# Kernel tuning notes

Measured on AMD Instinct MI355X. Metric: run time of the kernel, lower is better.

## Reference

```python
import jax, jax.numpy as jnp
import numpy as np

B, LC, LQ, D = 16, 1024, 128, 512


def setup_inputs() -> dict:
    key = jax.random.key(0)
    k1, k2, k3, k4, k5 = jax.random.split(key, 5)
    return {
        "C": jax.random.normal(k1, (B, LC, D), dtype=jnp.float32),
        "Q": jax.random.normal(k2, (B, LQ, D), dtype=jnp.float32),
        "Cmask": jax.random.randint(k3, (B, LC), 0, 2, dtype=jnp.int32),
        "Qmask": jax.random.randint(k4, (B, LQ), 0, 2, dtype=jnp.int32),
        "w_sim": jax.random.normal(k5, (3 * D,), dtype=jnp.float32) * (1.0 / np.sqrt(3 * D)),
    }


def reference(C, Q, Cmask, Qmask, w_sim):
    d = C.shape[-1]
    # Decompose Linear(3d -> 1) on cat([C_rep, Q_rep, C*Q]) into three dot products:
    # S[b,i,j] = C[b,i].w1 + Q[b,j].w2 + (C[b,i]*Q[b,j]).w3
    w1, w2, w3 = w_sim[:d], w_sim[d:2 * d], w_sim[2 * d:]
    s_c = C @ w1                                    # (B, Lc)
    s_q = Q @ w2                                    # (B, Lq)
    s_cq = jnp.einsum('bid,bjd->bij', C * w3, Q)    # (B, Lc, Lq)
    S = s_c[:, :, None] + s_q[:, None, :] + s_cq    # (B, Lc, Lq)

    NEG = jnp.asarray(-1e10, S.dtype)
    S1 = jax.nn.softmax(jnp.where(Qmask[:, None, :] != 0, NEG, S), axis=2)  # over question
    S2 = jax.nn.softmax(jnp.where(Cmask[:, :, None] != 0, NEG, S), axis=1)  # over context

    A = jnp.einsum('bij,bjd->bid', S1, Q)                       # (B, Lc, d)
    # bmm(bmm(S1, S2^T), C) == S1 @ (S2^T @ C) (associativity, avoids Lc x Lc)
    S2tC = jnp.einsum('bij,bid->bjd', S2, C)                    # (B, Lq, d)
    Bv = jnp.einsum('bij,bjd->bid', S1, S2tC)                   # (B, Lc, d)

    # dropout treated as identity (eval / p-effective 0) for the reference
    return jnp.concatenate([C, A, C * A, C * Bv], axis=2)       # (B, Lc, 4d)
```

## Files before the change

### kernel.cpp

```cpp
#include <hip/hip_runtime.h>
#include <hip/hip_bf16.h>
#include <math.h>

#define NB 16
#define NLC 1024
#define NLQ 128
#define ND 512
#define NEGV (-1.0e10f)

typedef __attribute__((ext_vector_type(8))) short bf16x8f;
typedef __attribute__((ext_vector_type(4))) float f32x4a;

__device__ inline unsigned short f2bf(float f) {
    unsigned u = __float_as_uint(f);
    unsigned r = (u + 0x7fffu + ((u >> 16) & 1u)) >> 16;
    return (unsigned short)r;
}

__device__ inline int xcd_swz(int bid, int nwg) {
    int chunk = nwg >> 3;
    return (bid & 7) * chunk + (bid >> 3);
}

__global__ __launch_bounds__(512) void k_prep2(const float* __restrict__ C,
                                               const float* __restrict__ Q,
                                               const float* __restrict__ w,
                                               unsigned short* __restrict__ Cw3,
                                               unsigned short* __restrict__ Ct,
                                               unsigned short* __restrict__ Qb,
                                               unsigned short* __restrict__ Qt,
                                               float* __restrict__ sc,
                                               float* __restrict__ sq) {
    __shared__ float T[64][65];
    int x = blockIdx.x, t = threadIdx.x;
    const float* src; const float* wdot; const float* wmul;
    unsigned short* rout; unsigned short* tout; float* sdst;
    int rows;
    if (x < 256) {
        int b = x >> 4, r0t = (x & 15) * 64;
        src = C + ((size_t)b * NLC + r0t) * ND;
        wdot = w; wmul = w + 2 * ND;
        rout = Cw3 + ((size_t)b * NLC + r0t) * ND;
        tout = Ct + (size_t)b * ND * NLC + r0t;
        sdst = sc + b * NLC + r0t;
        rows = NLC;
    } else {
        int x2 = x - 256;
        int b = x2 >> 1, r0t = (x2 & 1) * 64;
        src = Q + ((size_t)b * NLQ + r0t) * ND;
        wdot = w + ND; wmul = nullptr;
        rout = Qb + ((size_t)b * NLQ + r0t) * ND;
        tout = Qt + (size_t)b * ND * NLQ + r0t;
        sdst = sq + b * NLQ + r0t;
        rows = NLQ;
    }
    int r = t >> 3;
    int s8 = (t & 7) * 8;
    float dacc = 0.f;
    for (int c = 0; c < 8; ++c) {
        int dbase = c * 64 + s8;
        float4 v0 = *(const float4*)&src[(size_t)r * ND + dbase];
        float4 v1 = *(const float4*)&src[(size_t)r * ND + dbase + 4];
        float4 wd0 = *(const float4*)&wdot[dbase];
        float4 wd1 = *(const float4*)&wdot[dbase + 4];
        dacc += v0.x * wd0.x + v0.y * wd0.y + v0.z * wd0.z + v0.w * wd0.w;
        dacc += v1.x * wd1.x + v1.y * wd1.y + v1.z * wd1.z + v1.w * wd1.w;
        float f8[8] = {v0.x, v0.y, v0.z, v0.w, v1.x, v1.y, v1.z, v1.w};
        unsigned short o[8];
        if (wmul) {
            float4 w30 = *(const float4*)&wmul[dbase];
            float4 w31 = *(const float4*)&wmul[dbase + 4];
            float m8[8] = {w30.x, w30.y, w30.z, w30.w, w31.x, w31.y, w31.z, w31.w};
#pragma unroll
            for (int e = 0; e < 8; ++e) o[e] = f2bf(f8[e] * m8[e]);
        } else {
#pragma unroll
            for (int e = 0; e < 8; ++e) o[e] = f2bf(f8[e]);
        }
        *(int4*)&rout[(size_t)r * ND + dbase] = *(int4*)o;
#pragma unroll
        for (int e = 0; e < 8; ++e) T[r][s8 + e] = f8[e];
        __syncthreads();
        {
            int dd = t >> 3, seg = (t & 7) * 8;
            unsigned short o16[8];
#pragma unroll
            for (int e = 0; e < 8; ++e) o16[e] = f2bf(T[seg + e][dd]);
            *(int4*)&tout[(size_t)(c * 64 + dd) * rows + seg] = *(int4*)o16;
        }
        __syncthreads();
    }
    dacc += __shfl_xor(dacc, 1, 64);
    dacc += __shfl_xor(dacc, 2, 64);
    dacc += __shfl_xor(dacc, 4, 64);
    if ((t & 7) == 0) sdst[r] = dacc;
}

__global__ __launch_bounds__(256) void k_S(const unsigned short* __restrict__ Cw3,
                                           const unsigned short* __restrict__ Qb,
                                           const float* __restrict__ sc,
                                           const float* __restrict__ sq,
                                           const int* __restrict__ Qmask,
                                           const int* __restrict__ Cmask,
                                           unsigned short* __restrict__ P1,
                                           unsigned short* __restrict__ Eb,
                                           float* __restrict__ colm,
                                           float* __restrict__ cols) {
    __shared__ __align__(16) char lds[25088];
    int lg = xcd_swz(blockIdx.x, 256);
    int b = lg >> 4, it = lg & 15, i0 = it * 64;
    int t = threadIdx.x, lane = t & 63, wv = t >> 6;
    int g = lane >> 4, r16 = lane & 15;
    const unsigned short* Asrc = Cw3 + ((size_t)b * NLC + i0) * ND;
    const unsigned short* Bsrc = Qb + (size_t)b * NLQ * ND;
    f32x4a zero = {0.f, 0.f, 0.f, 0.f};
    f32x4a acc[8];
#pragma unroll
    for (int nf = 0; nf < 8; ++nf) acc[nf] = zero;

    for (int kk = 0; kk < 8; ++kk) {
#pragma unroll
        for (int p = 0; p < 2; ++p) {
            int u = t + p * 256;
            int i = u >> 3, db = u & 7;
            int4 v = *(const int4*)(Asrc + (size_t)i * ND + kk * 64 + db * 8);
            *(int4*)(lds + i * 128 + ((db * 16) ^ ((i & 7) << 4))) = v;
        }
#pragma unroll
        for (int p = 0; p < 4; ++p) {
            int u = t + p * 256;
            int j = u >> 3, db = u & 7;
            int4 v = *(const int4*)(Bsrc + (size_t)j * ND + kk * 64 + db * 8);
            *(int4*)(lds + 8192 + j * 128 + ((db * 16) ^ ((j & 7) << 4))) = v;
        }
        __syncthreads();
#pragma unroll
        for (int ks = 0; ks < 2; ++ks) {
            int inner = ks * 64 + g * 16;
            bf16x8f a = *(const bf16x8f*)(lds + (16 * wv + r16) * 128 + (inner ^ ((r16 & 7) << 4)));
#pragma unroll
            for (int nf = 0; nf < 8; ++nf) {
                bf16x8f bq = *(const bf16x8f*)(lds + 8192 + (16 * nf + r16) * 128 + (inner ^ ((r16 & 7) << 4)));
                acc[nf] = __builtin_amdgcn_mfma_f32_16x16x32_bf16(a, bq, acc[nf], 0, 0, 0);
            }
        }
        __syncthreads();
    }

    const float* scp = sc + b * NLC + i0;
    const float* sqp = sq + b * NLQ;
    const int* qm = Qmask + b * NLQ;
    const int* cmb = Cmask + b * NLC;
    float sv[8][4];
    float scr[4];
#pragma unroll
    for (int reg = 0; reg < 4; ++reg) scr[reg] = scp[16 * wv + 4 * g + reg];
    int qmv[8];
#pragma unroll
    for (int nf = 0; nf < 8; ++nf) {
        qmv[nf] = qm[16 * nf + r16];
        float sqv = sqp[16 * nf + r16];
#pragma unroll
        for (int reg = 0; reg < 4; ++reg) sv[nf][reg] = acc[nf][reg] + scr[reg] + sqv;
    }

    unsigned short* P1p = P1 + ((size_t)b * NLC + i0) * NLQ;
#pragma unroll
    for (int reg = 0; reg < 4; ++reg) {
        float m = -INFINITY;
#pragma unroll
        for (int nf = 0; nf < 8; ++nf) m = fmaxf(m, qmv[nf] ? NEGV : sv[nf][reg]);
#pragma unroll
        for (int off = 8; off >= 1; off >>= 1) m = fmaxf(m, __shfl_xor(m, off, 64));
        float pv[8], s = 0.f;
#pragma unroll
        for (int nf = 0; nf < 8; ++nf) {
            pv[nf] = __expf((qmv[nf] ? NEGV : sv[nf][reg]) - m);
            s += pv[nf];
        }
#pragma unroll
        for (int off = 8; off >= 1; off >>= 1) s += __shfl_xor(s, off, 64);
        float rsi = 1.0f / s;
        int i = 16 * wv + 4 * g + reg;
#pragma unroll
        for (int nf = 0; nf < 8; ++nf)
            P1p[(size_t)i * NLQ + 16 * nf + r16] = f2bf(pv[nf] * rsi);
    }

    int cmv[4];
#pragma unroll
    for (int reg = 0; reg < 4; ++reg) cmv[reg] = cmb[i0 + 16 * wv + 4 * g + reg];
    float vm2[8][4];
#pragma unroll
    for (int nf = 0; nf < 8; ++nf)
#pragma unroll
        for (int reg = 0; reg < 4; ++reg) vm2[nf][reg] = cmv[reg] ? NEGV : sv[nf][reg];

    float* cpm = (float*)(lds + 20480);
    float* cps = (float*)(lds + 22528);
    float* mtl = (float*)(lds + 24576);
    float cm8[8], cs8[8];
#pragma unroll
    for (int nf = 0; nf < 8; ++nf) {
        float m = vm2[nf][0];
#pragma unroll
        for (int reg = 1; reg < 4; ++reg) m = fmaxf(m, vm2[nf][reg]);
        float s = 0.f;
#pragma unroll
        for (int reg = 0; reg < 4; ++reg) s += __expf(vm2[nf][reg] - m);
#pragma unroll
        for (int off = 16; off <= 32; off <<= 1) {
            float mo = __shfl_xor(m, off, 64);
            float so = __shfl_xor(s, off, 64);
            float mn = fmaxf(m, mo);
            s = s * __expf(m - mn) + so * __expf(mo - mn);
            m = mn;
        }
        cm8[nf] = m; cs8[nf] = s;
    }
    if (g == 0) {
#pragma unroll
        for (int nf = 0; nf < 8; ++nf) {
            cpm[(wv * 8 + nf) * 16 + r16] = cm8[nf];
            cps[(wv * 8 + nf) * 16 + r16] = cs8[nf];
        }
    }
    __syncthreads();
    if (t < 128) {
        int j = t, nf = j >> 4, rr = j & 15;
        float M = cpm[(0 * 8 + nf) * 16 + rr];
        float S = cps[(0 * 8 + nf) * 16 + rr];
#pragma unroll
        for (int w2 = 1; w2 < 4; ++w2) {
            float mo = cpm[(w2 * 8 + nf) * 16 + rr];
            float so = cps[(w2 * 8 + nf) * 16 + rr];
            float mn = fmaxf(M, mo);
            S = S * __expf(M - mn) + so * __expf(mo - mn);
            M = mn;
        }
        colm[((size_t)b * 16 + it) * NLQ + j] = M;
        cols[((size_t)b * 16 + it) * NLQ + j] = S;
        mtl[j] = M;
    }
    __syncthreads();

    unsigned short* ex = (unsigned short*)lds;
#pragma unroll
    for (int nf = 0; nf < 8; ++nf) {
        float mj = mtl[16 * nf + r16];
        unsigned short e4[4];
#pragma unroll
        for (int reg = 0; reg < 4; ++reg) e4[reg] = f2bf(__expf(vm2[nf][reg] - mj));
        *(uint2*)&ex[(16 * nf + r16) * 80 + 16 * wv + 4 * g] = *(uint2*)e4;
    }
    __syncthreads();
    {
        int j = t >> 1, half = t & 1;
        unsigned short* Ep = Eb + ((size_t)b * NLQ + j) * NLC + i0 + half * 32;
#pragma unroll
        for (int c = 0; c < 4; ++c)
            *(int4*)&Ep[c * 8] = *(int4*)&ex[j * 80 + half * 32 + c * 8];
    }
}

__global__ __launch_bounds__(256) void k_s2tc(const unsigned short* __restrict__ Eb,
                                              const unsigned short* __restrict__ Ct,
                                              const float* __restrict__ colm,
                                              const float* __restrict__ cols,
                                              float* __restrict__ pbuf) {
    __shared__ __align__(16) char lds[23552];
    int lg = xcd_swz(blockIdx.x, 512);
    int b = lg >> 5, kc = (lg >> 3) & 3, dt = lg & 7;
    int t = threadIdx.x, lane = t & 63, wv = t >> 6, g = lane >> 4, r16 = lane & 15;
    float* fb = (float*)lds;

    if (t < 128) {
        int j = t;
        const float* cmp = colm + (size_t)b * 16 * NLQ + j;
        const float* csp = cols + (size_t)b * 16 * NLQ + j;
        float M = -INFINITY;
#pragma unroll
        for (int p = 0; p < 16; ++p) M = fmaxf(M, cmp[p * NLQ]);
        float S = 0.f;
#pragma unroll
        for (int p = 0; p < 16; ++p) S += csp[p * NLQ] * __expf(cmp[p * NLQ] - M);
        float inv = 1.0f / S;
#pragma unroll
        for (int p = 0; p < 16; ++p) fb[p * NLQ + j] = __expf(cmp[p * NLQ] - M) * inv;
    }
    __syncthreads();

    const unsigned short* Ebb = Eb + (size_t)b * NLQ * NLC;
    const unsigned short* Ctb = Ct + ((size_t)b * ND + dt * 64) * NLC;
    f32x4a zero = {0.f, 0.f, 0.f, 0.f};
    f32x4a acc2[2][4], V[2][4];
#pragma unroll
    for (int mf = 0; mf < 2; ++mf)
#pragma unroll
        for (int nf = 0; nf < 4; ++nf) { acc2[mf][nf] = zero; V[mf][nf] = zero; }

    for (int ib = kc * 256; ib < kc * 256 + 256; ib += 32) {
#pragma unroll
        for (int p = 0; p < 2; ++p) {
            int u = t + p * 256;
            int j = u >> 2, c8 = (u & 3) * 8;
            int4 v = *(const int4*)(Ebb + (size_t)j * NLC + ib + c8);
            *(int4*)(lds + 8192 + (j * 40 + c8) * 2) = v;
        }
        {
            int dd = t >> 2, c8 = (t & 3) * 8;
            int4 v = *(const int4*)(Ctb + (size_t)dd * NLC + ib + c8);
            *(int4*)(lds + 18432 + (dd * 40 + c8) * 2) = v;
        }
        __syncthreads();
#pragma unroll
        for (int mf = 0; mf < 2; ++mf) {
            bf16x8f a = *(const bf16x8f*)(lds + 8192 + ((32 * wv + 16 * mf + r16) * 40 + g * 8) * 2);
#pragma unroll
            for (int nf = 0; nf < 4; ++nf) {
                bf16x8f bb = *(const bf16x8f*)(lds + 18432 + ((16 * nf + r16) * 40 + g * 8) * 2);
                acc2[mf][nf] = __builtin_amdgcn_mfma_f32_16x16x32_bf16(a, bb, acc2[mf][nf], 0, 0, 0);
            }
        }
        __syncthreads();
        if (ib & 32) {
            int itg = ib >> 6;
#pragma unroll
            for (int mf = 0; mf < 2; ++mf) {
                f32x4a f4 = *(const f32x4a*)(lds + (itg * NLQ + 32 * wv + 16 * mf + 4 * g) * 4);
#pragma unroll
                for (int nf = 0; nf < 4; ++nf) {
#pragma unroll
                    for (int reg = 0; reg < 4; ++reg)
                        V[mf][nf][reg] += f4[reg] * acc2[mf][nf][reg];
                    acc2[mf][nf] = zero;
                }
            }
        }
    }
    float* pb = pbuf + (((size_t)kc * NB + b) * ND + dt * 64) * NLQ;
#pragma unroll
    for (int mf = 0; mf < 2; ++mf)
#pragma unroll
        for (int nf = 0; nf < 4; ++nf) {
            float4 v;
            v.x = V[mf][nf][0]; v.y = V[mf][nf][1];
            v.z = V[mf][nf][2]; v.w = V[mf][nf][3];
            *(float4*)&pb[(size_t)(16 * nf + r16) * NLQ + 32 * wv + 16 * mf + 4 * g] = v;
        }
}

__global__ __launch_bounds__(256) void k_red(const float* __restrict__ pbuf,
                                             unsigned short* __restrict__ Vt) {
    size_t u = (size_t)blockIdx.x * 256 + threadIdx.x;
    const size_t cs = (size_t)NB * ND * NLQ;
    float4 s = *(const float4*)&pbuf[u * 4];
#pragma unroll
    for (int c = 1; c < 4; ++c) {
        float4 v = *(const float4*)&pbuf[cs * c + u * 4];
        s.x += v.x; s.y += v.y; s.z += v.z; s.w += v.w;
    }
    unsigned short o[4] = {f2bf(s.x), f2bf(s.y), f2bf(s.z), f2bf(s.w)};
    *(uint2*)&Vt[u * 4] = *(uint2*)o;
}

__global__ __launch_bounds__(256) void k_out(const unsigned short* __restrict__ P1,
                                             const unsigned short* __restrict__ Qt,
                                             const unsigned short* __restrict__ Vt,
                                             const float* __restrict__ C,
                                             float* __restrict__ Out) {
    __shared__ __align__(16) char lds[49152];
    int lg = xcd_swz(blockIdx.x, 2048);
    int b = lg >> 7, rem = lg & 127, it = rem >> 3, dt = rem & 7;
    int i0 = it * 64, d0 = dt * 64;
    int t = threadIdx.x, lane = t & 63, wv = t >> 6, g = lane >> 4, r16 = lane & 15;
    const unsigned short* P1b = P1 + ((size_t)b * NLC + i0) * NLQ;
    const unsigned short* Qtb = Qt + ((size_t)b * ND + d0) * NLQ;
    const unsigned short* Vtb = Vt + ((size_t)b * ND + d0) * NLQ;
#pragma unroll
    for (int p = 0; p < 4; ++p) {
        int u = t + p * 256;
        int r = u >> 4, c = u & 15;
        int swz = (c * 16) ^ ((r & 7) << 4);
        *(int4*)(lds + r * 256 + swz) = *(const int4*)(P1b + (size_t)r * NLQ + c * 8);
        *(int4*)(lds + 16384 + r * 256 + swz) = *(const int4*)(Qtb + (size_t)r * NLQ + c * 8);
        *(int4*)(lds + 32768 + r * 256 + swz) = *(const int4*)(Vtb + (size_t)r * NLQ + c * 8);
    }
    __syncthreads();
    f32x4a zero = {0.f, 0.f, 0.f, 0.f};
    f32x4a accA[4], accB[4];
#pragma unroll
    for (int nf = 0; nf < 4; ++nf) { accA[nf] = zero; accB[nf] = zero; }
#pragma unroll
    for (int ks = 0; ks < 4; ++ks) {
        int inner = ks * 64 + g * 16;
        bf16x8f a = *(const bf16x8f*)(lds + (16 * wv + r16) * 256 + (inner ^ ((r16 & 7) << 4)));
#pragma unroll
        for (int nf = 0; nf < 4; ++nf) {
            int ro = (16 * nf + r16) * 256 + (inner ^ ((r16 & 7) << 4));
            bf16x8f q = *(const bf16x8f*)(lds + 16384 + ro);
            accA[nf] = __builtin_amdgcn_mfma_f32_16x16x32_bf16(a, q, accA[nf], 0, 0, 0);
            bf16x8f vv = *(const bf16x8f*)(lds + 32768 + ro);
            accB[nf] = __builtin_amdgcn_mfma_f32_16x16x32_bf16(a, vv, accB[nf], 0, 0, 0);
        }
    }
    __syncthreads();

    float* At = (float*)lds;
    float* Bt = (float*)(lds + 17408);
#pragma unroll
    for (int nf = 0; nf < 4; ++nf) {
        int dloc = 16 * nf + r16;
#pragma unroll
        for (int reg = 0; reg < 4; ++reg) {
            int iloc = 16 * wv + 4 * g + reg;
            At[iloc * 68 + dloc] = accA[nf][reg];
            Bt[iloc * 68 + dloc] = accB[nf][reg];
        }
    }
    __syncthreads();

    const float* Cb = C + ((size_t)b * NLC + i0) * ND + d0;
    float* Ob = Out + ((size_t)b * NLC + i0) * (4 * ND);
#pragma unroll
    for (int p = 0; p < 4; ++p) {
        int u = t + p * 256;
        int row = u >> 4, c4 = (u & 15) * 4;
        float4 cv = *(const float4*)&Cb[(size_t)row * ND + c4];
        float4 av = *(const float4*)&At[row * 68 + c4];
        float4 bv = *(const float4*)&Bt[row * 68 + c4];
        float4 ca, cb;
        ca.x = cv.x * av.x; ca.y = cv.y * av.y; ca.z = cv.z * av.z; ca.w = cv.w * av.w;
        cb.x = cv.x * bv.x; cb.y = cv.y * bv.y; cb.z = cv.z * bv.z; cb.w = cv.w * bv.w;
        float* orow = Ob + (size_t)row * (4 * ND);
        *(float4*)&orow[d0 + c4] = cv;
        *(float4*)&orow[ND + d0 + c4] = av;
        *(float4*)&orow[2 * ND + d0 + c4] = ca;
        *(float4*)&orow[3 * ND + d0 + c4] = cb;
    }
}

extern "C" void kernel_launch(void* const* d_in, const int* in_sizes, int n_in,
                              void* d_out, int out_size, void* d_ws, size_t ws_size,
                              hipStream_t stream) {
    const float* C = (const float*)d_in[0];
    const float* Q = (const float*)d_in[1];
    const int* Cmask = (const int*)d_in[2];
    const int* Qmask = (const int*)d_in[3];
    const float* w = (const float*)d_in[4];
    float* out = (float*)d_out;

    char* ob = (char*)d_out;
    unsigned short* Cw3 = (unsigned short*)(ob + 0);
    unsigned short* Ct  = (unsigned short*)(ob + 16777216);
    unsigned short* Eb  = (unsigned short*)(ob + 33554432);
    unsigned short* Qb  = (unsigned short*)(ob + 37748736);
    float*          colm = (float*)(ob + 39845888);
    float*          colsv = (float*)(ob + 39976960);
    float*          pbuf = (float*)(ob + 40108032);

    char* wb = (char*)d_ws;
    float* sc = (float*)(wb + 0);
    float* sq = (float*)(wb + 65536);
    unsigned short* P1 = (unsigned short*)(wb + 73728);
    unsigned short* Qt = (unsigned short*)(wb + 4268032);
    unsigned short* Vt = (unsigned short*)(wb + 6365184);

    k_prep2<<<dim3(288), dim3(512), 0, stream>>>(C, Q, w, Cw3, Ct, Qb, Qt, sc, sq);
    k_S<<<dim3(256), dim3(256), 0, stream>>>(Cw3, Qb, sc, sq, Qmask, Cmask, P1, Eb, colm, colsv);
    k_s2tc<<<dim3(512), dim3(256), 0, stream>>>(Eb, Ct, colm, colsv, pbuf);
    k_red<<<dim3(1024), dim3(256), 0, stream>>>(pbuf, Vt);
    k_out<<<dim3(2048), dim3(256), 0, stream>>>(P1, Qt, Vt, C, out);
}
```

Baseline: 80.21 us.

## Drop split-K in S2tC kernel, fuse reduction, and register-prefetch next tile

The S2^T·C kernel no longer splits the Lc reduction into four chunks. Each block now runs the full 1024-long loop and writes the bf16 Vt result directly, which removes the separate k_red kernel and the fp32 partial buffer round trip. The global loads for the next 32-wide tile are issued into registers before the MFMA work on the current tile, giving simple software pipelining. The cost is that the grid shrinks from 512 to 128 blocks, which risks underfilling the GPU's compute units and leaves a longer serial loop per block.

Result: no change. 80.51 us (+0.4%).

```diff
diff --git a/kernel.cpp b/kernel.cpp
--- a/kernel.cpp
+++ b/kernel.cpp
@@ -267,10 +267,10 @@
                                               const unsigned short* __restrict__ Ct,
                                               const float* __restrict__ colm,
                                               const float* __restrict__ cols,
-                                              float* __restrict__ pbuf) {
+                                              unsigned short* __restrict__ Vt) {
     __shared__ __align__(16) char lds[23552];
-    int lg = xcd_swz(blockIdx.x, 512);
-    int b = lg >> 5, kc = (lg >> 3) & 3, dt = lg & 7;
+    int lg = xcd_swz(blockIdx.x, 128);
+    int b = lg >> 3, dt = lg & 7;
     int t = threadIdx.x, lane = t & 63, wv = t >> 6, g = lane >> 4, r16 = lane & 15;
     float* fb = (float*)lds;
 
@@ -288,10 +288,13 @@
 #pragma unroll
         for (int p = 0; p < 16; ++p) fb[p * NLQ + j] = __expf(cmp[p * NLQ] - M) * inv;
     }
-    __syncthreads();
 
     const unsigned short* Ebb = Eb + (size_t)b * NLQ * NLC;
     const unsigned short* Ctb = Ct + ((size_t)b * ND + dt * 64) * NLC;
+    int ja0 = t >> 2, ca0 = (t & 3) * 8;
+    int ja1 = (t + 256) >> 2, ca1 = ((t + 256) & 3) * 8;
+    int db0 = t >> 2, cb0 = (t & 3) * 8;
+
     f32x4a zero = {0.f, 0.f, 0.f, 0.f};
     f32x4a acc2[2][4], V[2][4];
 #pragma unroll
@@ -299,20 +302,21 @@
 #pragma unroll
         for (int nf = 0; nf < 4; ++nf) { acc2[mf][nf] = zero; V[mf][nf] = zero; }
 
-    for (int ib = kc * 256; ib < kc * 256 + 256; ib += 32) {
-#pragma unroll
-        for (int p = 0; p < 2; ++p) {
-            int u = t + p * 256;
-            int j = u >> 2, c8 = (u & 3) * 8;
-            int4 v = *(const int4*)(Ebb + (size_t)j * NLC + ib + c8);
-            *(int4*)(lds + 8192 + (j * 40 + c8) * 2) = v;
-        }
-        {
-            int dd = t >> 2, c8 = (t & 3) * 8;
-            int4 v = *(const int4*)(Ctb + (size_t)dd * NLC + ib + c8);
-            *(int4*)(lds + 18432 + (dd * 40 + c8) * 2) = v;
-        }
-        __syncthreads();
+    int4 ra0 = *(const int4*)(Ebb + (size_t)ja0 * NLC + ca0);
+    int4 ra1 = *(const int4*)(Ebb + (size_t)ja1 * NLC + ca1);
+    int4 rb  = *(const int4*)(Ctb + (size_t)db0 * NLC + cb0);
+    __syncthreads();
+
+    for (int ib = 0; ib < NLC; ib += 32) {
+        *(int4*)(lds + 8192 + (ja0 * 40 + ca0) * 2) = ra0;
+        *(int4*)(lds + 8192 + (ja1 * 40 + ca1) * 2) = ra1;
+        *(int4*)(lds + 18432 + (db0 * 40 + cb0) * 2) = rb;
+        __syncthreads();
+        if (ib + 32 < NLC) {
+            ra0 = *(const int4*)(Ebb + (size_t)ja0 * NLC + ib + 32 + ca0);
+            ra1 = *(const int4*)(Ebb + (size_t)ja1 * NLC + ib + 32 + ca1);
+            rb  = *(const int4*)(Ctb + (size_t)db0 * NLC + ib + 32 + cb0);
+        }
 #pragma unroll
         for (int mf = 0; mf < 2; ++mf) {
             bf16x8f a = *(const bf16x8f*)(lds + 8192 + ((32 * wv + 16 * mf + r16) * 40 + g * 8) * 2);
@@ -338,30 +342,16 @@
             }
         }
     }
-    float* pb = pbuf + (((size_t)kc * NB + b) * ND + dt * 64) * NLQ;
+    unsigned short* vb = Vt + ((size_t)b * ND + dt * 64) * NLQ;
 #pragma unroll
     for (int mf = 0; mf < 2; ++mf)
 #pragma unroll
         for (int nf = 0; nf < 4; ++nf) {
-            float4 v;
-            v.x = V[mf][nf][0]; v.y = V[mf][nf][1];
-            v.z = V[mf][nf][2]; v.w = V[mf][nf][3];
-            *(float4*)&pb[(size_t)(16 * nf + r16) * NLQ + 32 * wv + 16 * mf + 4 * g] = v;
-        }
-}
-
-__global__ __launch_bounds__(256) void k_red(const float* __restrict__ pbuf,
-                                             unsigned short* __restrict__ Vt) {
-    size_t u = (size_t)blockIdx.x * 256 + threadIdx.x;
-    const size_t cs = (size_t)NB * ND * NLQ;
-    float4 s = *(const float4*)&pbuf[u * 4];
-#pragma unroll
-    for (int c = 1; c < 4; ++c) {
-        float4 v = *(const float4*)&pbuf[cs * c + u * 4];
-        s.x += v.x; s.y += v.y; s.z += v.z; s.w += v.w;
-    }
-    unsigned short o[4] = {f2bf(s.x), f2bf(s.y), f2bf(s.z), f2bf(s.w)};
-    *(uint2*)&Vt[u * 4] = *(uint2*)o;
+            unsigned short o[4];
+#pragma unroll
+            for (int reg = 0; reg < 4; ++reg) o[reg] = f2bf(V[mf][nf][reg]);
+            *(uint2*)&vb[(size_t)(16 * nf + r16) * NLQ + 32 * wv + 16 * mf + 4 * g] = *(uint2*)o;
+        }
 }
 
 __global__ __launch_bounds__(256) void k_out(const unsigned short* __restrict__ P1,
@@ -457,7 +447,6 @@
     unsigned short* Qb  = (unsigned short*)(ob + 37748736);
     float*          colm = (float*)(ob + 39845888);
     float*          colsv = (float*)(ob + 39976960);
-    float*          pbuf = (float*)(ob + 40108032);
 
     char* wb = (char*)d_ws;
     float* sc = (float*)(wb + 0);
@@ -468,7 +457,6 @@
 
     k_prep2<<<dim3(288), dim3(512), 0, stream>>>(C, Q, w, Cw3, Ct, Qb, Qt, sc, sq);
     k_S<<<dim3(256), dim3(256), 0, stream>>>(Cw3, Qb, sc, sq, Qmask, Cmask, P1, Eb, colm, colsv);
-    k_s2tc<<<dim3(512), dim3(256), 0, stream>>>(Eb, Ct, colm, colsv, pbuf);
-    k_red<<<dim3(1024), dim3(256), 0, stream>>>(pbuf, Vt);
+    k_s2tc<<<dim3(128), dim3(256), 0, stream>>>(Eb, Ct, colm, colsv, Vt);
     k_out<<<dim3(2048), dim3(256), 0, stream>>>(P1, Qt, Vt, C, out);
 }
```
